# Performance work log

Hardware: AMD Instinct MI355X
Metric: run time of the kernel (lower is better)

The kernel has to match this reference:

```python
import jax, jax.numpy as jnp
import numpy as np

ATTN_BLOCK_SIZE = 1024
NUM_BUCKETS = 32  # int(sqrt(1024))


def _bucket_index():
    # Static index matching the torch init:
    # arange2 = ((arange1 - indices) % S) // num_buckets, then pick columns arange(nb)*nb
    S, nb = ATTN_BLOCK_SIZE, NUM_BUCKETS
    ar = np.arange(S)
    a2 = ((ar[:, None] - ar[None, :]) % S) // nb          # (S, S), values in [0, nb)
    a2 = a2[:, np.arange(nb) * nb]                         # (S, nb)
    return jnp.asarray(a2, dtype=jnp.int32)


def _decay_sum(x, alpha, beta, past_steps):
    # result[t] = alpha * sum_{i=0}^{P-1} beta**i * x[t-1-i]  (zeros for t-1-i < 0)
    # == the torch pad-and-add loop, expressed as one causal depthwise conv.
    B, S, D = x.shape
    P = past_steps
    w = alpha * beta ** jnp.arange(P, dtype=x.dtype)       # (P,) decay weights
    k = jnp.broadcast_to(w[::-1][None, None, :], (D, 1, P))  # depthwise kernel (O=D, I/g=1, W=P)
    xc = jnp.transpose(x, (0, 2, 1))                       # (B, D, S)
    y = jax.lax.conv_general_dilated(
        xc, k, window_strides=(1,), padding=[(P, 0)],
        dimension_numbers=('NCW', 'OIW', 'NCW'), feature_group_count=D,
    )[..., :S]                                             # (B, D, S)
    return jnp.transpose(y, (0, 2, 1))                     # (B, S, D)


def setup_inputs() -> dict:
    key = jax.random.key(0)
    k1, k2, k3, k4, k5 = jax.random.split(key, 5)
    B, S, nb = 1024, ATTN_BLOCK_SIZE, NUM_BUCKETS
    return {
        "x": jax.random.normal(k1, (B, S, nb), dtype=jnp.float32),
        "alpha": jax.random.uniform(k2, (1,), dtype=jnp.float32),
        "beta": jax.random.uniform(k3, (1,), dtype=jnp.float32),
        "pos_fwd_param": jax.random.normal(k4, (1, nb), dtype=jnp.float32),
        "pos_bwd_param": jax.random.normal(k5, (1, nb), dtype=jnp.float32),
        "past_steps": 128,
    }


def reference(x, alpha, beta, pos_fwd_param, pos_bwd_param, past_steps):
    S = ATTN_BLOCK_SIZE
    result = _decay_sum(x, alpha, beta, past_steps)        # (B, S, nb)
    ones = jnp.ones((S, 1), dtype=x.dtype)
    pb_fwd = ones @ pos_fwd_param                          # (S, nb)
    pb_bwd = jnp.take_along_axis(ones @ pos_bwd_param, _bucket_index(), axis=-1)  # (S, nb)
    return result + pb_fwd + pb_bwd
```

## Files before the change

kernel.cpp:

```cpp
#include <hip/hip_runtime.h>


typedef float f32x4 __attribute__((ext_vector_type(4)));

constexpr int S    = 1024;
constexpr int D    = 32;
constexpr int CL   = 16;
constexpr int NCH  = S / CL;
constexpr int LAG  = 8;
constexpr int NTHR = NCH * (D / 4);

__global__ __launch_bounds__(NTHR, 4)
void attn_pred_kernel(const float* __restrict__ x,
                      const float* __restrict__ alpha_p,
                      const float* __restrict__ beta_p,
                      const float* __restrict__ pos_fwd,
                      const float* __restrict__ pos_bwd,
                      const int*   __restrict__ past_p,
                      float* __restrict__ out)
{
    __shared__ f32x4 sA[NCH][D / 4];
    __shared__ f32x4 sC[NCH][D / 4];

    const int tid  = threadIdx.x;
    const int b    = blockIdx.x;
    const int lane = tid & 63;
    const int wv   = tid >> 6;
    const int g    = lane >> 3;
    const int dg   = lane & 7;
    const int c    = g * 8 + wv;
    const int s0   = c * CL;

    const float alpha = alpha_p[0];
    const float beta  = beta_p[0];
    const int   P     = past_p[0];

    double bb = (double)beta, bpd = 1.0;
    for (int e = P; e; e >>= 1) { if (e & 1) bpd *= bb; bb *= bb; }
    const float bP = (float)bpd;
    double b16 = (double)beta;
    for (int i = 0; i < 4; ++i) b16 *= b16;
    const float bCL = (float)b16;

    const f32x4* xg = reinterpret_cast<const f32x4*>(x) + (size_t)b * S * (D / 4) + dg;

    f32x4 xr[CL];
    #pragma unroll
    for (int i = 0; i < CL; ++i)
        xr[i] = xg[(s0 + i) * (D / 4)];

    f32x4 A = {0.f, 0.f, 0.f, 0.f};
    #pragma unroll
    for (int i = 0; i < CL; ++i) {
        A.x = fmaf(beta, A.x, xr[i].x);
        A.y = fmaf(beta, A.y, xr[i].y);
        A.z = fmaf(beta, A.z, xr[i].z);
        A.w = fmaf(beta, A.w, xr[i].w);
    }
    sA[c][dg] = A;
    __syncthreads();

    if (tid < D / 4) {
        f32x4 run = {0.f, 0.f, 0.f, 0.f};
        for (int cc = 0; cc < NCH; ++cc) {
            sC[cc][tid] = run;
            const f32x4 Ac = sA[cc][tid];
            f32x4 z;
            if (cc >= LAG) {
                const f32x4 Al = sA[cc - LAG][tid];
                z.x = alpha * fmaf(-bP, Al.x, Ac.x);
                z.y = alpha * fmaf(-bP, Al.y, Ac.y);
                z.z = alpha * fmaf(-bP, Al.z, Ac.z);
                z.w = alpha * fmaf(-bP, Al.w, Ac.w);
            } else {
                z.x = alpha * Ac.x; z.y = alpha * Ac.y;
                z.z = alpha * Ac.z; z.w = alpha * Ac.w;
            }
            run.x = fmaf(bCL, run.x, z.x);
            run.y = fmaf(bCL, run.y, z.y);
            run.z = fmaf(bCL, run.z, z.z);
            run.w = fmaf(bCL, run.w, z.w);
        }
    }
    __syncthreads();
    f32x4 y = sC[c][dg];

    const int d0 = dg * 4;
    const int q  = c >> 1;
    const f32x4 pf = reinterpret_cast<const f32x4*>(pos_fwd)[dg];
    f32x4 add;
    add.x = pf.x + pos_bwd[(q - (d0 + 0)) & (D - 1)];
    add.y = pf.y + pos_bwd[(q - (d0 + 1)) & (D - 1)];
    add.z = pf.z + pos_bwd[(q - (d0 + 2)) & (D - 1)];
    add.w = pf.w + pos_bwd[(q - (d0 + 3)) & (D - 1)];

    const float aP   = alpha * bP;
    const float m    = (g > 0) ? -aP : 0.f;
    f32x4* og = reinterpret_cast<f32x4*>(out) + ((size_t)b * S + s0) * (D / 4) + dg;
    #pragma unroll
    for (int i = 0; i < CL; ++i) {
        f32x4 o;
        o.x = y.x + add.x; o.y = y.y + add.y;
        o.z = y.z + add.z; o.w = y.w + add.w;
        __builtin_nontemporal_store(o, &og[i * (D / 4)]);

        f32x4 xl;
        xl.x = __shfl_up(xr[i].x, 8);
        xl.y = __shfl_up(xr[i].y, 8);
        xl.z = __shfl_up(xr[i].z, 8);
        xl.w = __shfl_up(xr[i].w, 8);

        y.x = fmaf(beta, y.x, fmaf(alpha, xr[i].x, m * xl.x));
        y.y = fmaf(beta, y.y, fmaf(alpha, xr[i].y, m * xl.y));
        y.z = fmaf(beta, y.z, fmaf(alpha, xr[i].z, m * xl.z));
        y.w = fmaf(beta, y.w, fmaf(alpha, xr[i].w, m * xl.w));
    }
}

extern "C" void kernel_launch(void* const* d_in, const int* in_sizes, int n_in,
                              void* d_out, int out_size, void* d_ws, size_t ws_size,
                              hipStream_t stream) {
    const float* x  = (const float*)d_in[0];
    const float* al = (const float*)d_in[1];
    const float* be = (const float*)d_in[2];
    const float* pf = (const float*)d_in[3];
    const float* pb = (const float*)d_in[4];
    const int*   ps = (const int*)d_in[5];
    float* out = (float*)d_out;

    const int B = in_sizes[0] / (S * D);
    attn_pred_kernel<<<dim3(B), NTHR, 0, stream>>>(x, al, be, pf, pb, ps, out);
}
```

Baseline: 240.2 us.

## Process four batch rows per block with double-buffered register prefetch of next row

Each block now handles four batch rows instead of one, loading the next row's x values into a second register array while the current row runs its chunk-sum, scan and output phases. The intent is to hide global load latency behind the serial shared-memory scan and to amortize per-block setup such as the beta power computation and the positional-bias loads. This doubles register usage for x and lowers the launch_bounds occupancy hint from 4 to 2. Barriers become raw s_barrier with explicit lgkmcnt waits plus sched barriers.

```diff
diff --git a/kernel.cpp b/kernel.cpp
--- a/kernel.cpp
+++ b/kernel.cpp
@@ -9,21 +9,21 @@
 constexpr int NCH  = S / CL;
 constexpr int LAG  = 8;
 constexpr int NTHR = NCH * (D / 4);
+constexpr int ROWS = 4;
 
-__global__ __launch_bounds__(NTHR, 4)
+__global__ __launch_bounds__(NTHR, 2)
 void attn_pred_kernel(const float* __restrict__ x,
                       const float* __restrict__ alpha_p,
                       const float* __restrict__ beta_p,
                       const float* __restrict__ pos_fwd,
                       const float* __restrict__ pos_bwd,
                       const int*   __restrict__ past_p,
-                      float* __restrict__ out)
+                      float* __restrict__ out, int B)
 {
     __shared__ f32x4 sA[NCH][D / 4];
     __shared__ f32x4 sC[NCH][D / 4];
 
     const int tid  = threadIdx.x;
-    const int b    = blockIdx.x;
     const int lane = tid & 63;
     const int wv   = tid >> 6;
     const int g    = lane >> 3;
@@ -41,49 +41,8 @@
     double b16 = (double)beta;
     for (int i = 0; i < 4; ++i) b16 *= b16;
     const float bCL = (float)b16;
-
-    const f32x4* xg = reinterpret_cast<const f32x4*>(x) + (size_t)b * S * (D / 4) + dg;
-
-    f32x4 xr[CL];
-    #pragma unroll
-    for (int i = 0; i < CL; ++i)
-        xr[i] = xg[(s0 + i) * (D / 4)];
-
-    f32x4 A = {0.f, 0.f, 0.f, 0.f};
-    #pragma unroll
-    for (int i = 0; i < CL; ++i) {
-        A.x = fmaf(beta, A.x, xr[i].x);
-        A.y = fmaf(beta, A.y, xr[i].y);
-        A.z = fmaf(beta, A.z, xr[i].z);
-        A.w = fmaf(beta, A.w, xr[i].w);
-    }
-    sA[c][dg] = A;
-    __syncthreads();
-
-    if (tid < D / 4) {
-        f32x4 run = {0.f, 0.f, 0.f, 0.f};
-        for (int cc = 0; cc < NCH; ++cc) {
-            sC[cc][tid] = run;
-            const f32x4 Ac = sA[cc][tid];
-            f32x4 z;
-            if (cc >= LAG) {
-                const f32x4 Al = sA[cc - LAG][tid];
-                z.x = alpha * fmaf(-bP, Al.x, Ac.x);
-                z.y = alpha * fmaf(-bP, Al.y, Ac.y);
-                z.z = alpha * fmaf(-bP, Al.z, Ac.z);
-                z.w = alpha * fmaf(-bP, Al.w, Ac.w);
-            } else {
-                z.x = alpha * Ac.x; z.y = alpha * Ac.y;
-                z.z = alpha * Ac.z; z.w = alpha * Ac.w;
-            }
-            run.x = fmaf(bCL, run.x, z.x);
-            run.y = fmaf(bCL, run.y, z.y);
-            run.z = fmaf(bCL, run.z, z.z);
-            run.w = fmaf(bCL, run.w, z.w);
-        }
-    }
-    __syncthreads();
-    f32x4 y = sC[c][dg];
+    const float aP  = alpha * bP;
+    const float m   = (g > 0) ? -aP : 0.f;
 
     const int d0 = dg * 4;
     const int q  = c >> 1;
@@ -94,27 +53,92 @@
     add.z = pf.z + pos_bwd[(q - (d0 + 2)) & (D - 1)];
     add.w = pf.w + pos_bwd[(q - (d0 + 3)) & (D - 1)];
 
-    const float aP   = alpha * bP;
-    const float m    = (g > 0) ? -aP : 0.f;
-    f32x4* og = reinterpret_cast<f32x4*>(out) + ((size_t)b * S + s0) * (D / 4) + dg;
+    const size_t rowStride = (size_t)S * (D / 4);
+    const int    b0        = blockIdx.x * ROWS;
+    const f32x4* xg0 = reinterpret_cast<const f32x4*>(x)
+                       + (size_t)b0 * rowStride + dg;
+    f32x4*       og0 = reinterpret_cast<f32x4*>(out)
+                       + (size_t)b0 * rowStride + (size_t)s0 * (D / 4) + dg;
+
+    f32x4 xra[CL], xrb[CL];
+
     #pragma unroll
-    for (int i = 0; i < CL; ++i) {
-        f32x4 o;
-        o.x = y.x + add.x; o.y = y.y + add.y;
-        o.z = y.z + add.z; o.w = y.w + add.w;
-        __builtin_nontemporal_store(o, &og[i * (D / 4)]);
+    for (int i = 0; i < CL; ++i)
+        xra[i] = xg0[(s0 + i) * (D / 4)];
 
-        f32x4 xl;
-        xl.x = __shfl_up(xr[i].x, 8);
-        xl.y = __shfl_up(xr[i].y, 8);
-        xl.z = __shfl_up(xr[i].z, 8);
-        xl.w = __shfl_up(xr[i].w, 8);
+#define ROW_BODY(XR, XN, R)                                                      \
+  if (b0 + (R) < B) {                                                            \
+           \
+    if (((R) + 1 < ROWS) && (b0 + (R) + 1 < B)) {                                \
+      const f32x4* xgn = xg0 + ((R) + 1) * rowStride;                            \
+      _Pragma("unroll")                                                          \
+      for (int i = 0; i < CL; ++i) XN[i] = xgn[(s0 + i) * (D / 4)];              \
+    }                                                                            \
+           \
+    f32x4 A = {0.f, 0.f, 0.f, 0.f};                                              \
+    _Pragma("unroll")                                                            \
+    for (int i = 0; i < CL; ++i) {                                               \
+      A.x = fmaf(beta, A.x, XR[i].x);                                            \
+      A.y = fmaf(beta, A.y, XR[i].y);                                            \
+      A.z = fmaf(beta, A.z, XR[i].z);                                            \
+      A.w = fmaf(beta, A.w, XR[i].w);                                            \
+    }                                                                            \
+    sA[c][dg] = A;                                                               \
+    asm volatile("s_waitcnt lgkmcnt(0)" ::: "memory"); \
+    __builtin_amdgcn_s_barrier();                                                \
+    __builtin_amdgcn_sched_barrier(0);                                           \
+                         \
+    if (tid < D / 4) {                                                           \
+      f32x4 run = {0.f, 0.f, 0.f, 0.f};                                          \
+      for (int cc = 0; cc < NCH; ++cc) {                                         \
+        sC[cc][tid] = run;                                                       \
+        const f32x4 Ac = sA[cc][tid];                                            \
+        f32x4 z;                                                                 \
+        if (cc >= LAG) {                                                         \
+          const f32x4 Al = sA[cc - LAG][tid];                                    \
+          z.x = alpha * fmaf(-bP, Al.x, Ac.x);                                   \
+          z.y = alpha * fmaf(-bP, Al.y, Ac.y);                                   \
+          z.z = alpha * fmaf(-bP, Al.z, Ac.z);                                   \
+          z.w = alpha * fmaf(-bP, Al.w, Ac.w);                                   \
+        } else {                                                                 \
+          z.x = alpha * Ac.x; z.y = alpha * Ac.y;                                \
+          z.z = alpha * Ac.z; z.w = alpha * Ac.w;                                \
+        }                                                                        \
+        run.x = fmaf(bCL, run.x, z.x);                                           \
+        run.y = fmaf(bCL, run.y, z.y);                                           \
+        run.z = fmaf(bCL, run.z, z.z);                                           \
+        run.w = fmaf(bCL, run.w, z.w);                                           \
+      }                                                                          \
+    }                                                                            \
+    asm volatile("s_waitcnt lgkmcnt(0)" ::: "memory");                           \
+    __builtin_amdgcn_s_barrier();                                                \
+    __builtin_amdgcn_sched_barrier(0);                                           \
+    f32x4 y = sC[c][dg];                                                         \
+       \
+    f32x4* og = og0 + (R) * rowStride;                                           \
+    _Pragma("unroll")                                                            \
+    for (int i = 0; i < CL; ++i) {                                               \
+      f32x4 o;                                                                   \
+      o.x = y.x + add.x; o.y = y.y + add.y;                                      \
+      o.z = y.z + add.z; o.w = y.w + add.w;                                      \
+      __builtin_nontemporal_store(o, &og[i * (D / 4)]);                          \
+      f32x4 xl;                                                                  \
+      xl.x = __shfl_up(XR[i].x, 8);                                              \
+      xl.y = __shfl_up(XR[i].y, 8);                                              \
+      xl.z = __shfl_up(XR[i].z, 8);                                              \
+      xl.w = __shfl_up(XR[i].w, 8);                                              \
+      y.x = fmaf(beta, y.x, fmaf(alpha, XR[i].x, m * xl.x));                     \
+      y.y = fmaf(beta, y.y, fmaf(alpha, XR[i].y, m * xl.y));                     \
+      y.z = fmaf(beta, y.z, fmaf(alpha, XR[i].z, m * xl.z));                     \
+      y.w = fmaf(beta, y.w, fmaf(alpha, XR[i].w, m * xl.w));                     \
+    }                                                                            \
+  }
 
-        y.x = fmaf(beta, y.x, fmaf(alpha, xr[i].x, m * xl.x));
-        y.y = fmaf(beta, y.y, fmaf(alpha, xr[i].y, m * xl.y));
-        y.z = fmaf(beta, y.z, fmaf(alpha, xr[i].z, m * xl.z));
-        y.w = fmaf(beta, y.w, fmaf(alpha, xr[i].w, m * xl.w));
-    }
+    ROW_BODY(xra, xrb, 0)
+    ROW_BODY(xrb, xra, 1)
+    ROW_BODY(xra, xrb, 2)
+    ROW_BODY(xrb, xra, 3)
+#undef ROW_BODY
 }
 
 extern "C" void kernel_launch(void* const* d_in, const int* in_sizes, int n_in,
@@ -129,5 +153,6 @@
     float* out = (float*)d_out;
 
     const int B = in_sizes[0] / (S * D);
-    attn_pred_kernel<<<dim3(B), NTHR, 0, stream>>>(x, al, be, pf, pb, ps, out);
+    const int grid = (B + ROWS - 1) / ROWS;
+    attn_pred_kernel<<<dim3(grid), NTHR, 0, stream>>>(x, al, be, pf, pb, ps, out, B);
 }
```

After: 247.8 us. 3.2% more time.
